# Kernel tuning notes

Measured on AMD Instinct MI355X. Metric: run time of the kernel, lower is better.

The kernel has to match this reference:

```python
import jax, jax.numpy as jnp
import numpy as np

N = 2048   # nodes per graph
M = 64     # input feature dim (m)
H = 256    # hidden_dim
E = 65536  # directed edges per graph
B = 8      # batch of graphs
EPS = 1e-5


def setup_inputs() -> dict:
    key = jax.random.key(0)
    ks = jax.random.split(key, 24)
    def xavier(k, out_d, in_d):
        s = float(np.sqrt(6.0 / (in_d + out_d)))
        return jax.random.uniform(k, (out_d, in_d), minval=-s, maxval=s, dtype=jnp.float32)
    dims = [(H, M), (2 * H, H), (4 * H, 2 * H), (4 * H, 4 * H), (4 * H, 4 * H)]
    inp = {}
    for i, (o, ii) in enumerate(dims, start=1):
        inp[f"w{i}"] = xavier(ks[i], o, ii)
        inp[f"b{i}"] = jnp.zeros((o,), jnp.float32)
        inp[f"g{i}"] = jnp.ones((o,), jnp.float32)   # batchnorm gamma
        inp[f"be{i}"] = jnp.zeros((o,), jnp.float32)  # batchnorm beta
    inp["ln_g"] = jnp.ones((4 * H,), jnp.float32)
    inp["ln_b"] = jnp.zeros((4 * H,), jnp.float32)
    inp["x"] = jax.random.normal(ks[20], (B, N, M, 1), dtype=jnp.float32)
    inp["edge_index"] = jax.random.randint(ks[21], (2, E), 0, N, dtype=jnp.int64)
    return inp


def reference(x, edge_index,
              w1, b1, g1, be1,
              w2, b2, g2, be2,
              w3, b3, g3, be3,
              w4, b4, g4, be4,
              w5, b5, g5, be5,
              ln_g, ln_b):
    # GCN normalization with self-loops (PyG GCNConv default), shared across batch
    loop = jnp.arange(N, dtype=edge_index.dtype)
    src = jnp.concatenate([edge_index[0], loop])
    dst = jnp.concatenate([edge_index[1], loop])
    deg = jax.ops.segment_sum(jnp.ones(src.shape[0], jnp.float32), dst, num_segments=N)
    dinv = deg ** -0.5
    norm = (dinv[src] * dinv[dst])[:, None]  # [E+N, 1]

    def gcn(h, w, b):
        h = h @ w.T                                        # [N, out]
        agg = jax.ops.segment_sum(h[src] * norm, dst, num_segments=N)
        return agg + b

    def bn(h, g, be):  # batchnorm over nodes (training stats, biased var)
        mu = h.mean(axis=0)
        var = ((h - mu) ** 2).mean(axis=0)
        return (h - mu) * jax.lax.rsqrt(var + EPS) * g + be

    def layer(h, w, b, g, be):
        return bn(jax.nn.leaky_relu(gcn(h, w, b), 0.01), g, be)

    def per_graph(xg):  # xg: [N, M, 1]
        h = xg[..., 0]
        h = layer(h, w1, b1, g1, be1)
        h = layer(h, w2, b2, g2, be2)
        h = layer(h, w3, b3, g3, be3)
        h = layer(h, w4, b4, g4, be4)
        h = layer(h, w5, b5, g5, be5)
        mu = h.mean(axis=-1, keepdims=True)
        var = ((h - mu) ** 2).mean(axis=-1, keepdims=True)
        h = (h - mu) * jax.lax.rsqrt(var + EPS) * ln_g + ln_b
        return h.reshape(-1)  # [N * 4H]

    return jax.vmap(per_graph)(x)  # [B, N*4H]
```

## Files before the change

kernel.cpp:

```cpp
#include <hip/hip_runtime.h>

#define NN 2048
#define EE 65536
#define BB 8
#define EPSF 1e-5f

typedef _Float16 f16;
typedef __attribute__((ext_vector_type(4))) _Float16 f16x4;
typedef __attribute__((ext_vector_type(8))) _Float16 f16x8;
typedef __attribute__((ext_vector_type(4))) float f32x4;
typedef __attribute__((ext_vector_type(4))) int i32x4;
typedef __attribute__((ext_vector_type(8))) short short8;
typedef __attribute__((ext_vector_type(4))) unsigned short u16x4;

__device__ inline unsigned short f2bf(float f) {
    unsigned u = __float_as_uint(f);
    unsigned r = (u + 0x7fffu + ((u >> 16) & 1u)) >> 16;
    return (unsigned short)r;
}

__device__ inline void gload16(const unsigned short* g, unsigned short* l) {
    __builtin_amdgcn_global_load_lds(
        (const __attribute__((address_space(1))) void*)g,
        (__attribute__((address_space(3))) void*)l, 16, 0, 0);
}

__global__ void setup_zero(int* __restrict__ counts, int* __restrict__ fillc,
                           float* __restrict__ bnsum, float* __restrict__ bnsq) {
    int i = blockIdx.x * 256 + threadIdx.x;
    if (i < NN) { counts[i] = 0; fillc[i] = 0; }
    if (i < 5 * BB * 1024) { bnsum[i] = 0.f; bnsq[i] = 0.f; }
}

__global__ void count_kernel(const int* __restrict__ ei, int* __restrict__ counts) {
    int e = blockIdx.x * 256 + threadIdx.x;
    if (e < EE + NN) {
        int d = (e < EE) ? ei[EE + e] : (e - EE);
        atomicAdd(&counts[d], 1);
    }
}

__global__ void dinv_kernel(const int* __restrict__ counts, float* __restrict__ dinv) {
    int i = blockIdx.x * 256 + threadIdx.x;
    if (i < NN) dinv[i] = rsqrtf((float)counts[i]);
}

__global__ void scan_kernel(const int* __restrict__ counts, int* __restrict__ row_ptr) {
    __shared__ int sh[256];
    int tid = threadIdx.x;
    int loc[8];
    int run = 0;
#pragma unroll
    for (int i = 0; i < 8; ++i) {
        loc[i] = run;
        run += (counts[tid * 8 + i] + 7) & ~7;
    }
    sh[tid] = run;
    __syncthreads();
    for (int off = 1; off < 256; off <<= 1) {
        int v = (tid >= off) ? sh[tid - off] : 0;
        __syncthreads();
        sh[tid] += v;
        __syncthreads();
    }
    int excl = sh[tid] - run;
#pragma unroll
    for (int i = 0; i < 8; ++i) row_ptr[tid * 8 + i] = excl + loc[i];
    if (tid == 255) row_ptr[NN] = excl + run;
}

__global__ void fill_pad(const int* __restrict__ ei, const float* __restrict__ dinv,
                         const int* __restrict__ row_ptr, const int* __restrict__ counts,
                         int* __restrict__ fillc, int* __restrict__ colA, float* __restrict__ valA) {
    int e = blockIdx.x * 256 + threadIdx.x;
    if (e < EE + NN) {
        int s, d;
        if (e < EE) { s = ei[e]; d = ei[EE + e]; }
        else        { s = d = e - EE; }
        int pos = row_ptr[d] + atomicAdd(&fillc[d], 1);
        colA[pos] = s;
        valA[pos] = dinv[s] * dinv[d];
    } else if (e < EE + 2 * NN) {
        int d = e - (EE + NN);
        int beg = row_ptr[d], end = row_ptr[d + 1];
        for (int k = counts[d]; k < end - beg; ++k) {
            colA[beg + k] = d;
            valA[beg + k] = 0.f;
        }
    }
}

__global__ void rowsum_kernel(const int* __restrict__ row_ptr, const float* __restrict__ valA,
                              float* __restrict__ R) {
    int d = blockIdx.x * 256 + threadIdx.x;
    if (d < NN) {
        float s = 0.f;
        for (int j = row_ptr[d]; j < row_ptr[d + 1]; ++j) s += valA[j];
        R[d] = s;
    }
}

#define WO1 16384
#define WO2 (WO1 + 131072)
#define WO3 (WO2 + 524288)
#define WO4 (WO3 + 1048576)
#define WO5 (WO4 + 1048576)
__global__ void conv_all(const float* __restrict__ s0, const float* __restrict__ s1,
                         const float* __restrict__ s2, const float* __restrict__ s3,
                         const float* __restrict__ s4, unsigned short* __restrict__ dst) {
    int i = blockIdx.x * 256 + threadIdx.x;
    if (i >= WO5) return;
    float v;
    if (i < WO1)      v = s0[i];
    else if (i < WO2) v = s1[i - WO1];
    else if (i < WO3) v = s2[i - WO2];
    else if (i < WO4) v = s3[i - WO3];
    else              v = s4[i - WO4];
    dst[i] = f2bf(v);
}

__global__ __launch_bounds__(256) void agg_f32(
    const float* __restrict__ Yin, const int* __restrict__ row_ptr,
    const int* __restrict__ colA, const float* __restrict__ valA,
    unsigned short* __restrict__ Aout) {
    constexpr int TPD = 16, DPB = 16, F = 64;
    int b = blockIdx.x & 7;
    int dst = (blockIdx.x >> 3) * DPB + threadIdx.x / TPD;
    int lane = threadIdx.x % TPD;
    const f32x4* Yb = (const f32x4*)(Yin + (size_t)b * NN * F);
    int beg = row_ptr[dst], end = row_ptr[dst + 1];
    f32x4 acc = {0.f, 0.f, 0.f, 0.f};
    for (int j = beg; j < end; j += 8) {
        i32x4 ca = *(const i32x4*)(colA + j);
        i32x4 cb = *(const i32x4*)(colA + j + 4);
        f32x4 va = *(const f32x4*)(valA + j);
        f32x4 vb = *(const f32x4*)(valA + j + 4);
        f32x4 y[8];
#pragma unroll
        for (int e = 0; e < 4; ++e) y[e] = Yb[(size_t)ca[e] * (F / 4) + lane];
#pragma unroll
        for (int e = 0; e < 4; ++e) y[4 + e] = Yb[(size_t)cb[e] * (F / 4) + lane];
#pragma unroll
        for (int e = 0; e < 8; ++e) {
            float ve = (e < 4) ? va[e] : vb[e - 4];
            acc += ve * y[e];
        }
    }
    u16x4 ob = {f2bf(acc[0]), f2bf(acc[1]), f2bf(acc[2]), f2bf(acc[3])};
    *(u16x4*)(Aout + (size_t)b * NN * F + (size_t)dst * F + lane * 4) = ob;
}

template <int F>
__global__ __launch_bounds__(256) void agg_mix(
    const f16* __restrict__ Yin, const int* __restrict__ row_ptr,
    const int* __restrict__ colA, const float* __restrict__ valA,
    const float* __restrict__ rowsumR, const float* __restrict__ s_arr,
    const float* __restrict__ t_arr, unsigned short* __restrict__ Aout) {
    constexpr int TPD = F / 8;
    constexpr int DPB = 256 / TPD;
    int b = blockIdx.x & 7;
    int dst = (blockIdx.x >> 3) * DPB + threadIdx.x / TPD;
    int lane = threadIdx.x % TPD;
    const f16* Yb = Yin + (size_t)b * NN * F;
    int beg = row_ptr[dst], end = row_ptr[dst + 1];
    float acc[8] = {};
    for (int j = beg; j < end; j += 8) {
        i32x4 ca = *(const i32x4*)(colA + j);
        i32x4 cb = *(const i32x4*)(colA + j + 4);
        f32x4 va = *(const f32x4*)(valA + j);
        f32x4 vb = *(const f32x4*)(valA + j + 4);
        f16x8 y[8];
#pragma unroll
        for (int e = 0; e < 4; ++e) y[e] = *(const f16x8*)(Yb + (size_t)ca[e] * F + lane * 8);
#pragma unroll
        for (int e = 0; e < 4; ++e) y[4 + e] = *(const f16x8*)(Yb + (size_t)cb[e] * F + lane * 8);
#pragma unroll
        for (int e = 0; e < 8; ++e) {
            float ve = (e < 4) ? va[e] : vb[e - 4];
#pragma unroll
            for (int k = 0; k < 8; ++k)
                acc[k] = __builtin_fmaf((float)y[e][k], ve, acc[k]);
        }
    }
    float R = rowsumR[dst];
    const float* sb = s_arr + b * F + lane * 8;
    const float* tb = t_arr + b * F + lane * 8;
    unsigned short ob[8];
#pragma unroll
    for (int k = 0; k < 8; ++k)
        ob[k] = f2bf(sb[k] * acc[k] + tb[k] * R);
    *(short8*)(Aout + (size_t)b * NN * F + (size_t)dst * F + lane * 8) = *(short8*)ob;
}

__global__ __launch_bounds__(256) void gemm_bias_lrelu(
    const unsigned short* __restrict__ A, const unsigned short* __restrict__ W,
    const float* __restrict__ bias, f16* __restrict__ Y,
    float* __restrict__ bnsum, float* __restrict__ bnsq, int K, int F) {
    __shared__ unsigned short lds_a[128 * 32];
    __shared__ unsigned short lds_b[128 * 32];
    const int tid = threadIdx.x;
    const int row0 = blockIdx.x * 128;
    const int col0 = blockIdx.y * 128;
    const int b = row0 >> 11;
    const int wave = tid >> 6;
    const int lane = tid & 63;
    const int wr = (wave >> 1) * 64;
    const int wc = (wave & 1) * 64;
    const int lrow = lane & 15;
    const int q = lane >> 4;
    const int lr = lane >> 2;
    const int lk = (lane & 3) * 8;

    f32x4 acc[4][4] = {};

    for (int k0 = 0; k0 < K; k0 += 32) {
#pragma unroll
        for (int t = 0; t < 2; ++t) {
            int r = wave * 32 + t * 16;
            gload16(A + (size_t)(row0 + r + lr) * K + k0 + lk, lds_a + r * 32);
            gload16(W + (size_t)(col0 + r + lr) * K + k0 + lk, lds_b + r * 32);
        }
        __syncthreads();
        short8 af[4], bf[4];
#pragma unroll
        for (int mt = 0; mt < 4; ++mt)
            af[mt] = *(const short8*)(lds_a + (wr + mt * 16 + lrow) * 32 + q * 8);
#pragma unroll
        for (int nt = 0; nt < 4; ++nt)
            bf[nt] = *(const short8*)(lds_b + (wc + nt * 16 + lrow) * 32 + q * 8);
#pragma unroll
        for (int mt = 0; mt < 4; ++mt)
#pragma unroll
            for (int nt = 0; nt < 4; ++nt)
                acc[mt][nt] = __builtin_amdgcn_mfma_f32_16x16x32_bf16(af[mt], bf[nt], acc[mt][nt], 0, 0, 0);
        __syncthreads();
    }
#pragma unroll
    for (int nt = 0; nt < 4; ++nt) {
        int col = col0 + wc + nt * 16 + lrow;
        float bv = bias[col];
        float s = 0.f, s2 = 0.f;
#pragma unroll
        for (int mt = 0; mt < 4; ++mt) {
#pragma unroll
            for (int reg = 0; reg < 4; ++reg) {
                int row = row0 + wr + mt * 16 + q * 4 + reg;
                float v = acc[mt][nt][reg] + bv;
                v = (v > 0.f) ? v : 0.01f * v;
                s += v;
                s2 += v * v;
                Y[(size_t)row * F + col] = (f16)v;
            }
        }
        s += __shfl_xor(s, 16);
        s2 += __shfl_xor(s2, 16);
        s += __shfl_xor(s, 32);
        s2 += __shfl_xor(s2, 32);
        if (q == 0) {
            atomicAdd(&bnsum[b * F + col], s);
            atomicAdd(&bnsq[b * F + col], s2);
        }
    }
}

__global__ void bn_finalize(const float* __restrict__ sum, const float* __restrict__ sq,
                            const float* __restrict__ g, const float* __restrict__ be,
                            float* __restrict__ s_arr, float* __restrict__ t_arr, int F) {
    int i = blockIdx.x * 256 + threadIdx.x;
    if (i >= BB * F) return;
    int c = i % F;
    float mu = sum[i] * (1.f / NN);
    float var = sq[i] * (1.f / NN) - mu * mu;
    float rs = rsqrtf(var + EPSF);
    float sc = g[c] * rs;
    s_arr[i] = sc;
    t_arr[i] = be[c] - mu * sc;
}

__global__ __launch_bounds__(256) void final_ln(const f16* __restrict__ Y,
                                                const float* __restrict__ s_arr, const float* __restrict__ t_arr,
                                                const float* __restrict__ lng, const float* __restrict__ lnb,
                                                float* __restrict__ out) {
    int bn = blockIdx.x;
    int b = bn >> 11;
    int tid = threadIdx.x;
    f16x4 hr = ((const f16x4*)(Y + (size_t)bn * 1024))[tid];
    f32x4 h = {(float)hr[0], (float)hr[1], (float)hr[2], (float)hr[3]};
    f32x4 sv = ((const f32x4*)(s_arr + b * 1024))[tid];
    f32x4 tv = ((const f32x4*)(t_arr + b * 1024))[tid];
    h = sv * h + tv;
    float s = h[0] + h[1] + h[2] + h[3];
    float s2 = h[0] * h[0] + h[1] * h[1] + h[2] * h[2] + h[3] * h[3];
#pragma unroll
    for (int off = 32; off; off >>= 1) {
        s += __shfl_down(s, off);
        s2 += __shfl_down(s2, off);
    }
    __shared__ float ssum[4], ssq[4];
    int wv = tid >> 6, ln = tid & 63;
    if (ln == 0) { ssum[wv] = s; ssq[wv] = s2; }
    __syncthreads();
    if (tid == 0) {
        float S = ssum[0] + ssum[1] + ssum[2] + ssum[3];
        float Q = ssq[0] + ssq[1] + ssq[2] + ssq[3];
        float mu = S * (1.f / 1024.f);
        float var = Q * (1.f / 1024.f) - mu * mu;
        ssum[0] = mu;
        ssq[0] = rsqrtf(var + EPSF);
    }
    __syncthreads();
    float mu = ssum[0], rs = ssq[0];
    f32x4 gv = ((const f32x4*)lng)[tid];
    f32x4 bv = ((const f32x4*)lnb)[tid];
    f32x4 o = (h - mu) * rs * gv + bv;
    ((f32x4*)(out + (size_t)bn * 1024))[tid] = o;
}

extern "C" void kernel_launch(void* const* d_in, const int* in_sizes, int n_in,
                              void* d_out, int out_size, void* d_ws, size_t ws_size,
                              hipStream_t stream) {
    const float* w[5]    = {(const float*)d_in[0], (const float*)d_in[4], (const float*)d_in[8],
                            (const float*)d_in[12], (const float*)d_in[16]};
    const float* bias[5] = {(const float*)d_in[1], (const float*)d_in[5], (const float*)d_in[9],
                            (const float*)d_in[13], (const float*)d_in[17]};
    const float* gam[5]  = {(const float*)d_in[2], (const float*)d_in[6], (const float*)d_in[10],
                            (const float*)d_in[14], (const float*)d_in[18]};
    const float* bet[5]  = {(const float*)d_in[3], (const float*)d_in[7], (const float*)d_in[11],
                            (const float*)d_in[15], (const float*)d_in[19]};
    const float* ln_g = (const float*)d_in[20];
    const float* ln_b = (const float*)d_in[21];
    const float* x    = (const float*)d_in[22];
    const int* ei     = (const int*)d_in[23];

    char* p = (char*)d_ws;
    auto alloc = [&](size_t bytes) {
        char* r = p;
        p += (bytes + 255) & ~(size_t)255;
        return r;
    };
    const int MAXE = EE + 8 * NN;
    float* dinv    = (float*)alloc(NN * 4);
    float* rowsumR = (float*)alloc(NN * 4);
    int* row_ptr   = (int*)alloc((NN + 1) * 4);
    int* counts    = (int*)alloc(NN * 4);
    int* fillc     = (int*)alloc(NN * 4);
    int* colA      = (int*)alloc((size_t)MAXE * 4);
    float* valA    = (float*)alloc((size_t)MAXE * 4);
    float* bnsum   = (float*)alloc((size_t)5 * BB * 1024 * 4);
    float* bnsq    = (float*)alloc((size_t)5 * BB * 1024 * 4);
    float* s_arr   = (float*)alloc((size_t)BB * 1024 * 4);
    float* t_arr   = (float*)alloc((size_t)BB * 1024 * 4);
    unsigned short* wbf = (unsigned short*)alloc((size_t)WO5 * 2);
    unsigned short* bufA = (unsigned short*)alloc((size_t)BB * NN * 1024 * 2);
    f16* bufY = (f16*)alloc((size_t)BB * NN * 1024 * 2);
    const int wofs[5] = {0, WO1, WO2, WO3, WO4};

    setup_zero<<<(5 * BB * 1024 + 255) / 256, 256, 0, stream>>>(counts, fillc, bnsum, bnsq);
    count_kernel<<<(EE + NN + 255) / 256, 256, 0, stream>>>(ei, counts);
    dinv_kernel<<<(NN + 255) / 256, 256, 0, stream>>>(counts, dinv);
    scan_kernel<<<1, 256, 0, stream>>>(counts, row_ptr);
    fill_pad<<<(EE + 2 * NN + 255) / 256, 256, 0, stream>>>(ei, dinv, row_ptr, counts, fillc, colA, valA);
    rowsum_kernel<<<(NN + 255) / 256, 256, 0, stream>>>(row_ptr, valA, rowsumR);
    conv_all<<<(WO5 + 255) / 256, 256, 0, stream>>>(w[0], w[1], w[2], w[3], w[4], wbf);

    const int Kin[5]  = {64, 256, 512, 1024, 1024};
    const int Fout[5] = {256, 512, 1024, 1024, 1024};
    for (int l = 0; l < 5; ++l) {
        int K = Kin[l], F = Fout[l];
        if (l == 0) {
            agg_f32<<<(NN / 16) * 8, 256, 0, stream>>>(x, row_ptr, colA, valA, bufA);
        } else {
            switch (K) {
                case 256:
                    agg_mix<256><<<(NN / 8) * 8, 256, 0, stream>>>(bufY, row_ptr, colA, valA, rowsumR, s_arr, t_arr, bufA);
                    break;
                case 512:
                    agg_mix<512><<<(NN / 4) * 8, 256, 0, stream>>>(bufY, row_ptr, colA, valA, rowsumR, s_arr, t_arr, bufA);
                    break;
                default:
                    agg_mix<1024><<<(NN / 2) * 8, 256, 0, stream>>>(bufY, row_ptr, colA, valA, rowsumR, s_arr, t_arr, bufA);
                    break;
            }
        }
        gemm_bias_lrelu<<<dim3(BB * NN / 128, F / 128), 256, 0, stream>>>(
            bufA, wbf + wofs[l], bias[l], bufY, bnsum + l * BB * 1024, bnsq + l * BB * 1024, K, F);
        bn_finalize<<<(BB * F + 255) / 256, 256, 0, stream>>>(
            bnsum + l * BB * 1024, bnsq + l * BB * 1024, gam[l], bet[l], s_arr, t_arr, F);
    }
    final_ln<<<BB * NN, 256, 0, stream>>>(bufY, s_arr, t_arr, ln_g, ln_b, (float*)d_out);
}
```

Before: 553.7 us.

## Use one wavefront per destination row in SpMM aggregation and fuse setup kernels

Replaces the aggregation kernel, which assigned F/8 threads per destination, with one 64-lane wavefront per destination row, each lane handling F/64 features. Neighbour indices and weights become wave-uniform scalar loads, which should cut redundant vector index loads and keep every lane on a single row. For F=1024 each lane now holds 16 features, which raises register use. The weight bf16 conversion kernel is also folded into the zeroing kernel to save a launch.

Result: no change. 554.5 us (+0.1%).

```diff
diff --git a/kernel.cpp b/kernel.cpp
--- a/kernel.cpp
+++ b/kernel.cpp
@@ -12,6 +12,7 @@
 typedef __attribute__((ext_vector_type(4))) int i32x4;
 typedef __attribute__((ext_vector_type(8))) short short8;
 typedef __attribute__((ext_vector_type(4))) unsigned short u16x4;
+typedef __attribute__((ext_vector_type(8))) unsigned short u16x8;
 
 __device__ inline unsigned short f2bf(float f) {
     unsigned u = __float_as_uint(f);
@@ -25,11 +26,29 @@
         (__attribute__((address_space(3))) void*)l, 16, 0, 0);
 }
 
-__global__ void setup_zero(int* __restrict__ counts, int* __restrict__ fillc,
-                           float* __restrict__ bnsum, float* __restrict__ bnsq) {
+#define WO1 16384
+#define WO2 (WO1 + 131072)
+#define WO3 (WO2 + 524288)
+#define WO4 (WO3 + 1048576)
+#define WO5 (WO4 + 1048576)
+
+__global__ void setup_conv(int* __restrict__ counts, int* __restrict__ fillc,
+                           float* __restrict__ bnsum, float* __restrict__ bnsq,
+                           const float* __restrict__ s0, const float* __restrict__ s1,
+                           const float* __restrict__ s2, const float* __restrict__ s3,
+                           const float* __restrict__ s4, unsigned short* __restrict__ dst) {
     int i = blockIdx.x * 256 + threadIdx.x;
     if (i < NN) { counts[i] = 0; fillc[i] = 0; }
     if (i < 5 * BB * 1024) { bnsum[i] = 0.f; bnsq[i] = 0.f; }
+    if (i < WO5) {
+        float v;
+        if (i < WO1)      v = s0[i];
+        else if (i < WO2) v = s1[i - WO1];
+        else if (i < WO3) v = s2[i - WO2];
+        else if (i < WO4) v = s3[i - WO3];
+        else              v = s4[i - WO4];
+        dst[i] = f2bf(v);
+    }
 }
 
 __global__ void count_kernel(const int* __restrict__ ei, int* __restrict__ counts) {
@@ -100,25 +119,6 @@
     }
 }
 
-#define WO1 16384
-#define WO2 (WO1 + 131072)
-#define WO3 (WO2 + 524288)
-#define WO4 (WO3 + 1048576)
-#define WO5 (WO4 + 1048576)
-__global__ void conv_all(const float* __restrict__ s0, const float* __restrict__ s1,
-                         const float* __restrict__ s2, const float* __restrict__ s3,
-                         const float* __restrict__ s4, unsigned short* __restrict__ dst) {
-    int i = blockIdx.x * 256 + threadIdx.x;
-    if (i >= WO5) return;
-    float v;
-    if (i < WO1)      v = s0[i];
-    else if (i < WO2) v = s1[i - WO1];
-    else if (i < WO3) v = s2[i - WO2];
-    else if (i < WO4) v = s3[i - WO3];
-    else              v = s4[i - WO4];
-    dst[i] = f2bf(v);
-}
-
 __global__ __launch_bounds__(256) void agg_f32(
     const float* __restrict__ Yin, const int* __restrict__ row_ptr,
     const int* __restrict__ colA, const float* __restrict__ valA,
@@ -150,46 +150,66 @@
     *(u16x4*)(Aout + (size_t)b * NN * F + (size_t)dst * F + lane * 4) = ob;
 }
 
+template <int PF>
+__device__ inline void ldrow(const f16* __restrict__ p, f16 (&y)[PF]) {
+    if constexpr (PF == 16) {
+        *(f16x8*)&y[0] = *(const f16x8*)p;
+        *(f16x8*)&y[8] = *(const f16x8*)(p + 8);
+    } else if constexpr (PF == 8) {
+        *(f16x8*)&y[0] = *(const f16x8*)p;
+    } else {
+        *(f16x4*)&y[0] = *(const f16x4*)p;
+    }
+}
+
 template <int F>
-__global__ __launch_bounds__(256) void agg_mix(
+__global__ __launch_bounds__(256) void agg_wave(
     const f16* __restrict__ Yin, const int* __restrict__ row_ptr,
     const int* __restrict__ colA, const float* __restrict__ valA,
     const float* __restrict__ rowsumR, const float* __restrict__ s_arr,
     const float* __restrict__ t_arr, unsigned short* __restrict__ Aout) {
-    constexpr int TPD = F / 8;
-    constexpr int DPB = 256 / TPD;
+    constexpr int PF = F / 64;
     int b = blockIdx.x & 7;
-    int dst = (blockIdx.x >> 3) * DPB + threadIdx.x / TPD;
-    int lane = threadIdx.x % TPD;
-    const f16* Yb = Yin + (size_t)b * NN * F;
+    int wv = __builtin_amdgcn_readfirstlane(threadIdx.x >> 6);
+    int dst = (blockIdx.x >> 3) * 4 + wv;
+    int lane = threadIdx.x & 63;
+    const f16* __restrict__ Yb = Yin + (size_t)b * NN * F;
     int beg = row_ptr[dst], end = row_ptr[dst + 1];
-    float acc[8] = {};
+    float acc[PF];
+#pragma unroll
+    for (int k = 0; k < PF; ++k) acc[k] = 0.f;
+
     for (int j = beg; j < end; j += 8) {
-        i32x4 ca = *(const i32x4*)(colA + j);
-        i32x4 cb = *(const i32x4*)(colA + j + 4);
-        f32x4 va = *(const f32x4*)(valA + j);
-        f32x4 vb = *(const f32x4*)(valA + j + 4);
-        f16x8 y[8];
-#pragma unroll
-        for (int e = 0; e < 4; ++e) y[e] = *(const f16x8*)(Yb + (size_t)ca[e] * F + lane * 8);
-#pragma unroll
-        for (int e = 0; e < 4; ++e) y[4 + e] = *(const f16x8*)(Yb + (size_t)cb[e] * F + lane * 8);
-#pragma unroll
-        for (int e = 0; e < 8; ++e) {
-            float ve = (e < 4) ? va[e] : vb[e - 4];
-#pragma unroll
-            for (int k = 0; k < 8; ++k)
-                acc[k] = __builtin_fmaf((float)y[e][k], ve, acc[k]);
-        }
-    }
+        int c[8];
+        float v[8];
+#pragma unroll
+        for (int e = 0; e < 8; ++e) { c[e] = colA[j + e]; v[e] = valA[j + e]; }
+        f16 y[8][PF];
+#pragma unroll
+        for (int e = 0; e < 8; ++e)
+            ldrow<PF>(Yb + (size_t)c[e] * F + lane * PF, y[e]);
+#pragma unroll
+        for (int e = 0; e < 8; ++e)
+#pragma unroll
+            for (int k = 0; k < PF; ++k)
+                acc[k] = __builtin_fmaf((float)y[e][k], v[e], acc[k]);
+    }
+
     float R = rowsumR[dst];
-    const float* sb = s_arr + b * F + lane * 8;
-    const float* tb = t_arr + b * F + lane * 8;
-    unsigned short ob[8];
-#pragma unroll
-    for (int k = 0; k < 8; ++k)
-        ob[k] = f2bf(sb[k] * acc[k] + tb[k] * R);
-    *(short8*)(Aout + (size_t)b * NN * F + (size_t)dst * F + lane * 8) = *(short8*)ob;
+    const float* sb = s_arr + b * F + lane * PF;
+    const float* tb = t_arr + b * F + lane * PF;
+    unsigned short ob[PF];
+#pragma unroll
+    for (int k = 0; k < PF; ++k) ob[k] = f2bf(sb[k] * acc[k] + tb[k] * R);
+    unsigned short* op = Aout + (size_t)b * NN * F + (size_t)dst * F + lane * PF;
+    if constexpr (PF == 16) {
+        *(u16x8*)op = *(u16x8*)&ob[0];
+        *(u16x8*)(op + 8) = *(u16x8*)&ob[8];
+    } else if constexpr (PF == 8) {
+        *(u16x8*)op = *(u16x8*)&ob[0];
+    } else {
+        *(u16x4*)op = *(u16x4*)&ob[0];
+    }
 }
 
 __global__ __launch_bounds__(256) void gemm_bias_lrelu(
@@ -355,13 +375,13 @@
     f16* bufY = (f16*)alloc((size_t)BB * NN * 1024 * 2);
     const int wofs[5] = {0, WO1, WO2, WO3, WO4};
 
-    setup_zero<<<(5 * BB * 1024 + 255) / 256, 256, 0, stream>>>(counts, fillc, bnsum, bnsq);
+    setup_conv<<<(WO5 + 255) / 256, 256, 0, stream>>>(counts, fillc, bnsum, bnsq,
+                                                      w[0], w[1], w[2], w[3], w[4], wbf);
     count_kernel<<<(EE + NN + 255) / 256, 256, 0, stream>>>(ei, counts);
     dinv_kernel<<<(NN + 255) / 256, 256, 0, stream>>>(counts, dinv);
     scan_kernel<<<1, 256, 0, stream>>>(counts, row_ptr);
     fill_pad<<<(EE + 2 * NN + 255) / 256, 256, 0, stream>>>(ei, dinv, row_ptr, counts, fillc, colA, valA);
     rowsum_kernel<<<(NN + 255) / 256, 256, 0, stream>>>(row_ptr, valA, rowsumR);
-    conv_all<<<(WO5 + 255) / 256, 256, 0, stream>>>(w[0], w[1], w[2], w[3], w[4], wbf);
 
     const int Kin[5]  = {64, 256, 512, 1024, 1024};
     const int Fout[5] = {256, 512, 1024, 1024, 1024};
@@ -372,13 +392,13 @@
         } else {
             switch (K) {
                 case 256:
-                    agg_mix<256><<<(NN / 8) * 8, 256, 0, stream>>>(bufY, row_ptr, colA, valA, rowsumR, s_arr, t_arr, bufA);
+                    agg_wave<256><<<(NN / 4) * 8, 256, 0, stream>>>(bufY, row_ptr, colA, valA, rowsumR, s_arr, t_arr, bufA);
                     break;
                 case 512:
-                    agg_mix<512><<<(NN / 4) * 8, 256, 0, stream>>>(bufY, row_ptr, colA, valA, rowsumR, s_arr, t_arr, bufA);
+                    agg_wave<512><<<(NN / 4) * 8, 256, 0, stream>>>(bufY, row_ptr, colA, valA, rowsumR, s_arr, t_arr, bufA);
                     break;
                 default:
-                    agg_mix<1024><<<(NN / 2) * 8, 256, 0, stream>>>(bufY, row_ptr, colA, valA, rowsumR, s_arr, t_arr, bufA);
+                    agg_wave<1024><<<(NN / 4) * 8, 256, 0, stream>>>(bufY, row_ptr, colA, valA, rowsumR, s_arr, t_arr, bufA);
                     break;
             }
         }
```
